# Optimization experiments

Hardware: AMD Instinct MI355X
Metric: run time of the kernel (lower is better)

## Reference

```python
import jax, jax.numpy as jnp
import numpy as np

S, P, H, E = 32, 32, 128, 64        # scenes, peds/scene, h_dim, embedding_dim
B1, B2 = 512, 1024                  # mlp_pre_pool hidden, bottleneck_dim
M1 = 1024                           # decoder mlp hidden
N = S * P
T = 12                              # seq_len (decode horizon)
BN_INV = 1.0 / np.sqrt(1.0 + 1e-5)  # eval-mode BatchNorm, running mean=0 var=1


def setup_inputs() -> dict:
    key = jax.random.key(0)
    ks = jax.random.split(key, 32)
    rn = lambda k, sh, s=0.05: jax.random.normal(k, sh, dtype=jnp.float32) * s
    inp = {
        'last_pos': rn(ks[0], (N, 2), 1.0),
        'last_pos_rel': rn(ks[1], (N, 2), 1.0),
        'h0': rn(ks[2], (N, H), 0.1),
        'c0': rn(ks[3], (N, H), 0.1),
        'seq_start_end': jnp.stack([jnp.arange(S) * P, (jnp.arange(S) + 1) * P], 1).astype(jnp.int32),
        # decoder spatial embedding Linear(2, E)
        'emb_W': rn(ks[4], (E, 2)), 'emb_b': rn(ks[5], (E,)),
        # LSTM (torch gate order i,f,g,o)
        'lstm_Wih': rn(ks[6], (4 * H, E)), 'lstm_Whh': rn(ks[7], (4 * H, H)),
        'lstm_bih': rn(ks[8], (4 * H,)), 'lstm_bhh': rn(ks[9], (4 * H,)),
        # hidden2pos Linear(H, 2)
        'pos_W': rn(ks[10], (2, H)), 'pos_b': rn(ks[11], (2,)),
        # pool_net spatial embedding Linear(2, E)
        'sp_W': rn(ks[12], (E, 2)), 'sp_b': rn(ks[13], (E,)),
        # mlp_pre_pool: Linear(E+H, 512)+BN+ReLU, Linear(512, 1024)+BN+ReLU
        'pp1_W': rn(ks[14], (B1, E + H)), 'pp1_b': rn(ks[15], (B1,)),
        'pp1_g': 1.0 + rn(ks[16], (B1,)), 'pp1_be': rn(ks[17], (B1,)),
        'pp2_W': rn(ks[18], (B2, B1)), 'pp2_b': rn(ks[19], (B2,)),
        'pp2_g': 1.0 + rn(ks[20], (B2,)), 'pp2_be': rn(ks[21], (B2,)),
        # decoder mlp: Linear(H+1024, 1024)+BN+ReLU, Linear(1024, H)+BN+ReLU
        'm1_W': rn(ks[22], (M1, H + B2)), 'm1_b': rn(ks[23], (M1,)),
        'm1_g': 1.0 + rn(ks[24], (M1,)), 'm1_be': rn(ks[25], (M1,)),
        'm2_W': rn(ks[26], (H, M1)), 'm2_b': rn(ks[27], (H,)),
        'm2_g': 1.0 + rn(ks[28], (H,)), 'm2_be': rn(ks[29], (H,)),
    }
    return inp


def _bn(x, g, b):
    return x * BN_INV * g + b


def reference(last_pos, last_pos_rel, h0, c0, seq_start_end,
              emb_W, emb_b, lstm_Wih, lstm_Whh, lstm_bih, lstm_bhh,
              pos_W, pos_b, sp_W, sp_b,
              pp1_W, pp1_b, pp1_g, pp1_be, pp2_W, pp2_b, pp2_g, pp2_be,
              m1_W, m1_b, m1_g, m1_be, m2_W, m2_b, m2_g, m2_be):
    # seq_start_end encodes uniform scenes of size P; pooling is done per scene.
    def step(carry, _):
        h, c, lp, din = carry  # h,c:[N,H]  lp:[N,2]  din:[N,E]
        gates = din @ lstm_Wih.T + lstm_bih + h @ lstm_Whh.T + lstm_bhh
        i, f, g_, o = jnp.split(gates, 4, axis=-1)
        c2 = jax.nn.sigmoid(f) * c + jax.nn.sigmoid(i) * jnp.tanh(g_)
        h2 = jax.nn.sigmoid(o) * jnp.tanh(c2)
        rel_pos = h2 @ pos_W.T + pos_b          # [N,2]
        curr = rel_pos + lp                     # [N,2]
        # ---- PoolHiddenNet: per-scene all-pairs gather -> MLP -> max ----
        ps = curr.reshape(S, P, 2)
        rel = ps[:, None, :, :] - ps[:, :, None, :]   # [s,i,j] = pos_j - pos_i
        rel = rel / jnp.maximum(jnp.linalg.norm(rel, axis=-1, keepdims=True), 1e-12)
        emb = rel @ sp_W.T + sp_b                      # [S,P,P,E]
        hj = jnp.broadcast_to(h2.reshape(S, 1, P, H), (S, P, P, H))
        x = jnp.concatenate([emb, hj], -1)             # [S,P,P,E+H]
        x = jax.nn.relu(_bn(x @ pp1_W.T + pp1_b, pp1_g, pp1_be))
        x = jax.nn.relu(_bn(x @ pp2_W.T + pp2_b, pp2_g, pp2_be))
        pool = x.max(axis=2).reshape(N, B2)            # max over neighbours j
        # ---- hidden refinement MLP ----
        dh = jnp.concatenate([h2, pool], 1)
        dh = jax.nn.relu(_bn(dh @ m1_W.T + m1_b, m1_g, m1_be))
        dh = jax.nn.relu(_bn(dh @ m2_W.T + m2_b, m2_g, m2_be))
        din2 = rel_pos @ emb_W.T + emb_b
        return (dh, c2, curr, din2), rel_pos

    din0 = last_pos_rel @ emb_W.T + emb_b
    _, preds = jax.lax.scan(step, (h0, c0, last_pos, din0), None, length=T)
    return preds  # [T, N, 2] predicted relative displacements
```

## Files before the change

### kernel.cpp

```cpp
#include <hip/hip_runtime.h>
#include <hip/hip_bf16.h>
#include <math.h>

#define DEVFN __device__ __forceinline__

constexpr float BN_INV = 0.99999500003749971f;

DEVFN float sigm(float x) { return 1.0f / (1.0f + expf(-x)); }

DEVFN unsigned short f2bf(float f) {
    __hip_bfloat16 b = __float2bfloat16(f);
    return *reinterpret_cast<unsigned short*>(&b);
}
DEVFN float bf2f(unsigned short u) {
    unsigned int x = ((unsigned int)u) << 16;
    return *reinterpret_cast<float*>(&x);
}
DEVFN void splitf(float v, unsigned short& h, unsigned short& l) {
    h = f2bf(v);
    l = f2bf(v - bf2f(h));
}
DEVFN unsigned int pack2(unsigned short a, unsigned short b) {
    return (unsigned int)a | ((unsigned int)b << 16);
}

typedef __attribute__((ext_vector_type(8))) short short8;
typedef __attribute__((ext_vector_type(4))) float f32x4;

#define ASYNC_COPY16(gsrc, ldst)                                                            \
    __builtin_amdgcn_global_load_lds((const __attribute__((address_space(1))) unsigned int*)(gsrc), \
                                     (__attribute__((address_space(3))) unsigned int*)(ldst), 16, 0, 0)


__global__ void pre_lstm(const float* __restrict__ Wih, const float* __restrict__ Whh,
                         const float* __restrict__ bih, const float* __restrict__ bhh,
                         float* __restrict__ WgT, float* __restrict__ bg) {
    int idx = blockIdx.x * blockDim.x + threadIdx.x;
    int k = idx >> 9, t = idx & 511;
    WgT[idx] = (k < 64) ? Wih[t * 64 + k] : Whh[t * 128 + (k - 64)];
    if (idx < 512) bg[idx] = bih[idx] + bhh[idx];
}

__global__ void pre_wh1(const float* __restrict__ pp1W, const float* __restrict__ pp1g,
                        float* __restrict__ Wh1T) {
    int idx = blockIdx.x * blockDim.x + threadIdx.x;
    int h = idx >> 9, k = idx & 511;
    Wh1T[idx] = pp1W[k * 192 + 64 + h] * (BN_INV * pp1g[k]);
}

__global__ void pre_mp(const float* __restrict__ spW, const float* __restrict__ spb,
                       const float* __restrict__ pp1W, const float* __restrict__ pp1b,
                       const float* __restrict__ pp1g, const float* __restrict__ pp1be,
                       float* __restrict__ Mp, float* __restrict__ c1) {
    int k = blockIdx.x * blockDim.x + threadIdx.x;
    float m0 = 0.f, m1 = 0.f, c0 = 0.f;
    for (int e = 0; e < 64; e++) {
        float w = pp1W[k * 192 + e];
        m0 += spW[e * 2] * w; m1 += spW[e * 2 + 1] * w; c0 += spb[e] * w;
    }
    float s = BN_INV * pp1g[k];
    Mp[k] = m0 * s; Mp[512 + k] = m1 * s;
    c1[k] = (c0 + pp1b[k]) * s + pp1be[k];
}

__global__ void pre_w2bf(const float* __restrict__ W, const float* __restrict__ b,
                         const float* __restrict__ g, const float* __restrict__ be,
                         unsigned short* __restrict__ Wbf, float* __restrict__ cv, int swz) {
    int idx = blockIdx.x * blockDim.x + threadIdx.x;
    int ko = idx >> 9, k = idx & 511;
    float s = BN_INV * g[ko];
    int outk = swz ? ((k & ~63) | ((((k >> 3) & 7) ^ (ko & 7)) << 3) | (k & 7)) : k;
    Wbf[(ko << 9) + outk] = f2bf(W[idx] * s);
    if (idx < 1024) cv[idx] = b[idx] * s + be[idx];
}

__global__ void pre_w1split(const float* __restrict__ W, const float* __restrict__ b,
                            const float* __restrict__ g, const float* __restrict__ be,
                            unsigned short* __restrict__ Wh, unsigned short* __restrict__ Wl,
                            float* __restrict__ cv) {
    int idx = blockIdx.x * blockDim.x + threadIdx.x;
    int ko = idx / 1152;
    float s = BN_INV * g[ko];
    unsigned short h, l;
    splitf(W[idx] * s, h, l);
    Wh[idx] = h; Wl[idx] = l;
    if (idx < 1024) {
        float s2 = BN_INV * g[idx];
        cv[idx] = b[idx] * s2 + be[idx];
    }
}

__global__ void pre_w2split(const float* __restrict__ W, const float* __restrict__ b,
                            const float* __restrict__ g, const float* __restrict__ be,
                            unsigned short* __restrict__ Wh, unsigned short* __restrict__ Wl,
                            float* __restrict__ cv) {
    int idx = blockIdx.x * blockDim.x + threadIdx.x;
    int ko = idx >> 10;
    float s = BN_INV * g[ko];
    unsigned short h, l;
    splitf(W[idx] * s, h, l);
    Wh[idx] = h; Wl[idx] = l;
    if (idx < 128) {
        float s2 = BN_INV * g[idx];
        cv[idx] = b[idx] * s2 + be[idx];
    }
}

__global__ void pre_init(const float* __restrict__ lp, const float* __restrict__ lpr,
                         const float* __restrict__ h0, const float* __restrict__ c0,
                         const float* __restrict__ embW, const float* __restrict__ embb,
                         float* __restrict__ h_st, float* __restrict__ c_st,
                         float* __restrict__ curr, float* __restrict__ din) {
    int idx = blockIdx.x * blockDim.x + threadIdx.x;
    h_st[idx] = h0[idx];
    c_st[idx] = c0[idx];
    if (idx < 1024 * 2) curr[idx] = lp[idx];
    if (idx < 1024 * 64) {
        int n = idx >> 6, e = idx & 63;
        din[idx] = fmaf(lpr[n * 2], embW[e * 2], fmaf(lpr[n * 2 + 1], embW[e * 2 + 1], embb[e]));
    }
}


__global__ __launch_bounds__(512) void k_lstm(
    const float* __restrict__ WgT, const float* __restrict__ bg,
    float* __restrict__ h_st, float* __restrict__ c_st,
    float* __restrict__ din, float* __restrict__ curr,
    unsigned short* __restrict__ h2h, unsigned short* __restrict__ h2l,
    const float* __restrict__ posW, const float* __restrict__ posb,
    const float* __restrict__ embW, const float* __restrict__ embb,
    const float* __restrict__ Wh1T, const float* __restrict__ c1,
    float* __restrict__ Hp, int doHp,
    float* __restrict__ preds) {
    int n0 = blockIdx.x << 2;
    int t = threadIdx.x;
    __shared__ float xs[4][256];
    __shared__ float gates[4][512];
    __shared__ float h2s[4][128];
    __shared__ float rp[4][2];
#pragma unroll
    for (int u = 0; u < 2; u++) {
        int lin = t + (u << 9);
        int r = lin >> 8, k = lin & 255;
        float v = 0.f;
        if (k < 64) v = din[(n0 + r) * 64 + k];
        else if (k < 192) v = h_st[(n0 + r) * 128 + (k - 64)];
        xs[r][k] = v;
    }
    __syncthreads();
    float a0 = bg[t], a1 = a0, a2 = a0, a3 = a0;
#pragma unroll 4
    for (int k = 0; k < 192; k++) {
        float w = WgT[(k << 9) + t];
        a0 = fmaf(xs[0][k], w, a0);
        a1 = fmaf(xs[1][k], w, a1);
        a2 = fmaf(xs[2][k], w, a2);
        a3 = fmaf(xs[3][k], w, a3);
    }
    gates[0][t] = a0; gates[1][t] = a1; gates[2][t] = a2; gates[3][t] = a3;
    __syncthreads();
    {
        int r = t >> 7, hx = t & 127;
        float ig = sigm(gates[r][hx]);
        float fg = sigm(gates[r][128 + hx]);
        float gg = tanhf(gates[r][256 + hx]);
        float og = sigm(gates[r][384 + hx]);
        float c2 = fmaf(fg, c_st[(n0 + r) * 128 + hx], ig * gg);
        float h2 = og * tanhf(c2);
        c_st[(n0 + r) * 128 + hx] = c2;
        unsigned short sh, sl;
        splitf(h2, sh, sl);
        h2h[(n0 + r) * 128 + hx] = sh;
        h2l[(n0 + r) * 128 + hx] = sl;
        h2s[r][hx] = h2;
    }
    __syncthreads();
    int wv = t >> 6, l = t & 63;
    if (wv < 4) {
        float p0 = fmaf(h2s[wv][l], posW[l], h2s[wv][l + 64] * posW[l + 64]);
        float p1 = fmaf(h2s[wv][l], posW[128 + l], h2s[wv][l + 64] * posW[192 + l]);
#pragma unroll
        for (int off = 32; off > 0; off >>= 1) {
            p0 += __shfl_down(p0, off, 64);
            p1 += __shfl_down(p1, off, 64);
        }
        if (l == 0) { rp[wv][0] = p0 + posb[0]; rp[wv][1] = p1 + posb[1]; }
    }
    __syncthreads();
    if (t < 256) {
        int r = t >> 6, e = t & 63;
        float r0 = rp[r][0], r1 = rp[r][1];
        din[(n0 + r) * 64 + e] = fmaf(r0, embW[e * 2], fmaf(r1, embW[e * 2 + 1], embb[e]));
        if (e == 0) {
            preds[(n0 + r) * 2] = r0; preds[(n0 + r) * 2 + 1] = r1;
            curr[(n0 + r) * 2] += r0; curr[(n0 + r) * 2 + 1] += r1;
        }
    }
    if (doHp) {
        float cc = c1[t];
        float q0 = cc, q1 = cc, q2 = cc, q3 = cc;
#pragma unroll 4
        for (int h = 0; h < 128; h++) {
            float w = Wh1T[(h << 9) + t];
            q0 = fmaf(h2s[0][h], w, q0);
            q1 = fmaf(h2s[1][h], w, q1);
            q2 = fmaf(h2s[2][h], w, q2);
            q3 = fmaf(h2s[3][h], w, q3);
        }
        Hp[((n0 + 0) << 9) + t] = q0;
        Hp[((n0 + 1) << 9) + t] = q1;
        Hp[((n0 + 2) << 9) + t] = q2;
        Hp[((n0 + 3) << 9) + t] = q3;
    }
}

__global__ __launch_bounds__(256) void k_x1(
    const float* __restrict__ Hp, const float* __restrict__ Mp,
    const float* __restrict__ curr, unsigned short* __restrict__ x1g) {
    int bid = blockIdx.x;
    int c = bid & 7, q = bid >> 3;
    int i = q & 31, g = q >> 5;
    int s = (g << 3) + c;
    int si = (s << 5) + i;
    int t = threadIdx.x;
    __shared__ float rx[32], ry[32];
    __shared__ float m0s[512], m1s[512];
    for (int u = t; u < 512; u += 256) { m0s[u] = Mp[u]; m1s[u] = Mp[512 + u]; }
    if (t < 32) {
        int jg = (s << 5) + t;
        float dx = curr[jg * 2] - curr[si * 2];
        float dy = curr[jg * 2 + 1] - curr[si * 2 + 1];
        float den = fmaxf(sqrtf(dx * dx + dy * dy), 1e-12f);
        rx[t] = dx / den; ry[t] = dy / den;
    }
    __syncthreads();
    int j = t >> 3, c8 = t & 7;
    float rxv = rx[j], ryv = ry[j];
    const float* hp = Hp + (((s << 5) + j) << 9);
    unsigned short* op = x1g + ((size_t)((si << 5) + j) << 9);
    int swz = (c8 ^ (j & 7)) << 3;
#pragma unroll
    for (int kt = 0; kt < 512; kt += 64) {
        int k = kt + (c8 << 3);
        float4 ha = *(const float4*)(hp + k);
        float4 hb = *(const float4*)(hp + k + 4);
        uint4 o;
        o.x = pack2(f2bf(fmaxf(fmaf(rxv, m0s[k + 0], fmaf(ryv, m1s[k + 0], ha.x)), 0.f)),
                    f2bf(fmaxf(fmaf(rxv, m0s[k + 1], fmaf(ryv, m1s[k + 1], ha.y)), 0.f)));
        o.y = pack2(f2bf(fmaxf(fmaf(rxv, m0s[k + 2], fmaf(ryv, m1s[k + 2], ha.z)), 0.f)),
                    f2bf(fmaxf(fmaf(rxv, m0s[k + 3], fmaf(ryv, m1s[k + 3], ha.w)), 0.f)));
        o.z = pack2(f2bf(fmaxf(fmaf(rxv, m0s[k + 4], fmaf(ryv, m1s[k + 4], hb.x)), 0.f)),
                    f2bf(fmaxf(fmaf(rxv, m0s[k + 5], fmaf(ryv, m1s[k + 5], hb.y)), 0.f)));
        o.w = pack2(f2bf(fmaxf(fmaf(rxv, m0s[k + 6], fmaf(ryv, m1s[k + 6], hb.z)), 0.f)),
                    f2bf(fmaxf(fmaf(rxv, m0s[k + 7], fmaf(ryv, m1s[k + 7], hb.w)), 0.f)));
        *(uint4*)(op + kt + swz) = o;
    }
}

__global__ __launch_bounds__(1024, 4) void k_pool_g(
    const unsigned short* __restrict__ x1g, const unsigned short* __restrict__ W2bf,
    const float* __restrict__ c2v,
    unsigned short* __restrict__ poolh, unsigned short* __restrict__ pooll) {
    int bid = blockIdx.x;
    int c = bid & 7, q = bid >> 3;
    int inner = q & 15, g = q >> 4;
    int s = (g << 3) + c;
    int rb = inner >> 2;
    int koB = (inner & 3) << 8;
    int t = threadIdx.x;
    int lane = t & 63, wv = t >> 6;
    int quad = lane >> 4, l15 = lane & 15;
    int wr = wv >> 2, wc = wv & 3;
    int qrow = wr << 6, qcol = wc << 6;
    __shared__ unsigned short As[256 * 64];
    __shared__ unsigned short Bs[256 * 64];
    f32x4 acc[4][4];
#pragma unroll
    for (int a = 0; a < 4; a++)
#pragma unroll
        for (int b = 0; b < 4; b++) acc[a][b] = (f32x4){0.f, 0.f, 0.f, 0.f};

    int rlane = lane >> 3;
    int clane = (lane & 7) << 3;
    const unsigned short* gA = x1g + (size_t)((s << 10) + (rb << 8) + (wv << 4) + rlane) * 512 + clane;
    const unsigned short* gB = W2bf + (size_t)(koB + (wv << 4) + rlane) * 512 + clane;
    unsigned short* lA = As + (wv << 10);
    unsigned short* lB = Bs + (wv << 10);
    const unsigned short* pa0 = As + ((qrow + l15) << 6) + ((quad ^ (l15 & 7)) << 3);
    const unsigned short* pb0 = Bs + ((qcol + l15) << 6) + ((quad ^ (l15 & 7)) << 3);
    const unsigned short* pa1 = As + ((qrow + l15) << 6) + (((4 + quad) ^ (l15 & 7)) << 3);
    const unsigned short* pb1 = Bs + ((qcol + l15) << 6) + (((4 + quad) ^ (l15 & 7)) << 3);

    for (int kt = 0; kt < 512; kt += 64) {
        ASYNC_COPY16(gA + kt, lA);
        ASYNC_COPY16(gA + kt + 8 * 512, lA + (8 << 6));
        ASYNC_COPY16(gB + kt, lB);
        ASYNC_COPY16(gB + kt + 8 * 512, lB + (8 << 6));
        __syncthreads();
        {
            short8 aF[4], bF[4];
#pragma unroll
            for (int a = 0; a < 4; a++) aF[a] = *(const short8*)(pa0 + (a << 10));
#pragma unroll
            for (int b = 0; b < 4; b++) bF[b] = *(const short8*)(pb0 + (b << 10));
#pragma unroll
            for (int a = 0; a < 4; a++)
#pragma unroll
                for (int b = 0; b < 4; b++)
                    acc[a][b] = __builtin_amdgcn_mfma_f32_16x16x32_bf16(aF[a], bF[b], acc[a][b], 0, 0, 0);
#pragma unroll
            for (int a = 0; a < 4; a++) aF[a] = *(const short8*)(pa1 + (a << 10));
#pragma unroll
            for (int b = 0; b < 4; b++) bF[b] = *(const short8*)(pb1 + (b << 10));
#pragma unroll
            for (int a = 0; a < 4; a++)
#pragma unroll
                for (int b = 0; b < 4; b++)
                    acc[a][b] = __builtin_amdgcn_mfma_f32_16x16x32_bf16(aF[a], bF[b], acc[a][b], 0, 0, 0);
        }
        __syncthreads();
    }

    float mx0[4], mx1[4];
#pragma unroll
    for (int b = 0; b < 4; b++) {
        float m = acc[0][b].x;
#pragma unroll
        for (int a = 0; a < 2; a++) {
            m = fmaxf(m, acc[a][b].x); m = fmaxf(m, acc[a][b].y);
            m = fmaxf(m, acc[a][b].z); m = fmaxf(m, acc[a][b].w);
        }
        m = fmaxf(m, __shfl_xor(m, 16));
        m = fmaxf(m, __shfl_xor(m, 32));
        mx0[b] = m;
        float n = acc[2][b].x;
#pragma unroll
        for (int a = 2; a < 4; a++) {
            n = fmaxf(n, acc[a][b].x); n = fmaxf(n, acc[a][b].y);
            n = fmaxf(n, acc[a][b].z); n = fmaxf(n, acc[a][b].w);
        }
        n = fmaxf(n, __shfl_xor(n, 16));
        n = fmaxf(n, __shfl_xor(n, 32));
        mx1[b] = n;
    }
    float v0 = (quad == 0) ? mx0[0] : (quad == 1) ? mx0[1] : (quad == 2) ? mx0[2] : mx0[3];
    float v1 = (quad == 0) ? mx1[0] : (quad == 1) ? mx1[1] : (quad == 2) ? mx1[2] : mx1[3];
    int col = koB + qcol + (quad << 4) + l15;
    int i0 = (rb << 3) + (wr << 1);
    int si0 = (s << 5) + i0;
    float bias = c2v[col];
    float w0 = fmaxf(v0 + bias, 0.f);
    float w1 = fmaxf(v1 + bias, 0.f);
    unsigned short h0, l0, h1, l1;
    splitf(w0, h0, l0); splitf(w1, h1, l1);
    poolh[si0 * 1024 + col] = h0; pooll[si0 * 1024 + col] = l0;
    poolh[(si0 + 1) * 1024 + col] = h1; pooll[(si0 + 1) * 1024 + col] = l1;
}

__global__ __launch_bounds__(256) void k_pool_mfma(
    const float* __restrict__ Hp, const float* __restrict__ Mp,
    const unsigned short* __restrict__ W2bf,
    const float* __restrict__ c2v, const float* __restrict__ curr,
    unsigned short* __restrict__ poolh, unsigned short* __restrict__ pooll) {
    int s = blockIdx.z;
    int rb = blockIdx.y;
    int koBase = blockIdx.x << 7;
    int t = threadIdx.x;
    int lane = t & 63, wv = t >> 6;
    int quad = lane >> 4, l15 = lane & 15;
    int qrow = (wv >> 1) << 6;
    int qcol = (wv & 1) << 6;

    __shared__ unsigned short As[128 * 40];
    __shared__ unsigned short Bs[128 * 40];
    __shared__ float rx[128], ry[128];

    if (t < 128) {
        int iL = t >> 5, j = t & 31;
        int ig = (s << 5) + (rb << 2) + iL;
        int jg = (s << 5) + j;
        float dx = curr[jg * 2] - curr[ig * 2];
        float dy = curr[jg * 2 + 1] - curr[ig * 2 + 1];
        float den = fmaxf(sqrtf(dx * dx + dy * dy), 1e-12f);
        rx[t] = dx / den; ry[t] = dy / den;
    }
    __syncthreads();

    f32x4 acc[4][4];
#pragma unroll
    for (int a = 0; a < 4; a++)
#pragma unroll
        for (int b = 0; b < 4; b++) acc[a][b] = (f32x4){0.f, 0.f, 0.f, 0.f};

    int r0 = t >> 3, c4 = (t & 7) << 2;
    int bn = t >> 1, bk = (t & 1) << 4;

    for (int kt = 0; kt < 512; kt += 32) {
#pragma unroll
        for (int p = 0; p < 4; p++) {
            int rr = r0 + (p << 5);
            int j = rr & 31;
            int kg = kt + c4;
            float4 hv = *(const float4*)(Hp + (((s << 5) + j) << 9) + kg);
            float4 m0 = *(const float4*)(Mp + kg);
            float4 m1 = *(const float4*)(Mp + 512 + kg);
            float rxv = rx[rr], ryv = ry[rr];
            float v0 = fmaxf(fmaf(rxv, m0.x, fmaf(ryv, m1.x, hv.x)), 0.f);
            float v1 = fmaxf(fmaf(rxv, m0.y, fmaf(ryv, m1.y, hv.y)), 0.f);
            float v2 = fmaxf(fmaf(rxv, m0.z, fmaf(ryv, m1.z, hv.z)), 0.f);
            float v3 = fmaxf(fmaf(rxv, m0.w, fmaf(ryv, m1.w, hv.w)), 0.f);
            unsigned int u0 = pack2(f2bf(v0), f2bf(v1));
            unsigned int u1 = pack2(f2bf(v2), f2bf(v3));
            *(uint2*)(&As[rr * 40 + c4]) = make_uint2(u0, u1);
        }
        {
            const unsigned short* src = W2bf + (((koBase + bn) << 9) + kt + bk);
            uint4 w0 = *(const uint4*)src;
            uint4 w1 = *(const uint4*)(src + 8);
            *(uint4*)(&Bs[bn * 40 + bk]) = w0;
            *(uint4*)(&Bs[bn * 40 + bk + 8]) = w1;
        }
        __syncthreads();
        short8 bF[4];
#pragma unroll
        for (int b = 0; b < 4; b++)
            bF[b] = *(const short8*)(&Bs[(qcol + (b << 4) + l15) * 40 + (quad << 3)]);
#pragma unroll
        for (int a = 0; a < 4; a++) {
            short8 aF = *(const short8*)(&As[(qrow + (a << 4) + l15) * 40 + (quad << 3)]);
#pragma unroll
            for (int b = 0; b < 4; b++)
                acc[a][b] = __builtin_amdgcn_mfma_f32_16x16x32_bf16(aF, bF[b], acc[a][b], 0, 0, 0);
        }
        __syncthreads();
    }

    float mx0[4], mx1[4];
#pragma unroll
    for (int b = 0; b < 4; b++) {
        float m = acc[0][b].x;
#pragma unroll
        for (int a = 0; a < 2; a++) {
            m = fmaxf(m, acc[a][b].x); m = fmaxf(m, acc[a][b].y);
            m = fmaxf(m, acc[a][b].z); m = fmaxf(m, acc[a][b].w);
        }
        m = fmaxf(m, __shfl_xor(m, 16));
        m = fmaxf(m, __shfl_xor(m, 32));
        mx0[b] = m;
        float n = acc[2][b].x;
#pragma unroll
        for (int a = 2; a < 4; a++) {
            n = fmaxf(n, acc[a][b].x); n = fmaxf(n, acc[a][b].y);
            n = fmaxf(n, acc[a][b].z); n = fmaxf(n, acc[a][b].w);
        }
        n = fmaxf(n, __shfl_xor(n, 16));
        n = fmaxf(n, __shfl_xor(n, 32));
        mx1[b] = n;
    }
    float v0 = (quad == 0) ? mx0[0] : (quad == 1) ? mx0[1] : (quad == 2) ? mx0[2] : mx0[3];
    float v1 = (quad == 0) ? mx1[0] : (quad == 1) ? mx1[1] : (quad == 2) ? mx1[2] : mx1[3];
    int col = koBase + qcol + (quad << 4) + l15;
    int i0 = (rb << 2) + ((wv >> 1) << 1);
    int si0 = (s << 5) + i0;
    float bias = c2v[col];
    float w0 = fmaxf(v0 + bias, 0.f);
    float w1 = fmaxf(v1 + bias, 0.f);
    unsigned short h0, l0, h1, l1;
    splitf(w0, h0, l0); splitf(w1, h1, l1);
    poolh[si0 * 1024 + col] = h0; pooll[si0 * 1024 + col] = l0;
    poolh[(si0 + 1) * 1024 + col] = h1; pooll[(si0 + 1) * 1024 + col] = l1;
}

__global__ __launch_bounds__(256) void k_m1_mfma(
    const unsigned short* __restrict__ h2h, const unsigned short* __restrict__ h2l,
    const unsigned short* __restrict__ poolh, const unsigned short* __restrict__ pooll,
    const unsigned short* __restrict__ M1h, const unsigned short* __restrict__ M1l,
    const float* __restrict__ cm1,
    unsigned short* __restrict__ dh1h, unsigned short* __restrict__ dh1l) {
    int rowBase = blockIdx.y << 6;
    int koBase = blockIdx.x << 6;
    int t = threadIdx.x;
    int lane = t & 63, wv = t >> 6;
    int quad = lane >> 4, l15 = lane & 15;
    int qrow = (wv >> 1) << 5, qcol = (wv & 1) << 5;
    __shared__ unsigned short Ah[64 * 40], Al[64 * 40], Bh[64 * 40], Bl[64 * 40];
    f32x4 acc[2][2];
#pragma unroll
    for (int a = 0; a < 2; a++)
#pragma unroll
        for (int b = 0; b < 2; b++) acc[a][b] = (f32x4){0.f, 0.f, 0.f, 0.f};

    int ar = t >> 2, ak = (t & 3) << 3;

    for (int kt = 0; kt < 1152; kt += 32) {
        {
            const unsigned short* sH;
            const unsigned short* sL;
            int off;
            if (kt < 128) {
                off = (rowBase + ar) * 128 + kt + ak;
                sH = h2h; sL = h2l;
            } else {
                off = (rowBase + ar) * 1024 + (kt - 128) + ak;
                sH = poolh; sL = pooll;
            }
            *(uint4*)&Ah[ar * 40 + ak] = *(const uint4*)(sH + off);
            *(uint4*)&Al[ar * 40 + ak] = *(const uint4*)(sL + off);
        }
        {
            int boff = (koBase + ar) * 1152 + kt + ak;
            *(uint4*)&Bh[ar * 40 + ak] = *(const uint4*)(M1h + boff);
            *(uint4*)&Bl[ar * 40 + ak] = *(const uint4*)(M1l + boff);
        }
        __syncthreads();
        short8 bH[2], bL[2];
#pragma unroll
        for (int b = 0; b < 2; b++) {
            int boff = (qcol + (b << 4) + l15) * 40 + (quad << 3);
            bH[b] = *(const short8*)(&Bh[boff]);
            bL[b] = *(const short8*)(&Bl[boff]);
        }
#pragma unroll
        for (int a = 0; a < 2; a++) {
            int aoff = (qrow + (a << 4) + l15) * 40 + (quad << 3);
            short8 aH = *(const short8*)(&Ah[aoff]);
            short8 aL = *(const short8*)(&Al[aoff]);
#pragma unroll
            for (int b = 0; b < 2; b++) {
                acc[a][b] = __builtin_amdgcn_mfma_f32_16x16x32_bf16(aH, bH[b], acc[a][b], 0, 0, 0);
                acc[a][b] = __builtin_amdgcn_mfma_f32_16x16x32_bf16(aH, bL[b], acc[a][b], 0, 0, 0);
                acc[a][b] = __builtin_amdgcn_mfma_f32_16x16x32_bf16(aL, bH[b], acc[a][b], 0, 0, 0);
            }
        }
        __syncthreads();
    }
#pragma unroll
    for (int b = 0; b < 2; b++) {
        int col = koBase + qcol + (b << 4) + l15;
        float bias = cm1[col];
#pragma unroll
        for (int a = 0; a < 2; a++) {
#pragma unroll
            for (int rg = 0; rg < 4; rg++) {
                int row = rowBase + qrow + (a << 4) + (quad << 2) + rg;
                float v = fmaxf(acc[a][b][rg] + bias, 0.f);
                unsigned short sh, sl;
                splitf(v, sh, sl);
                dh1h[row * 1024 + col] = sh;
                dh1l[row * 1024 + col] = sl;
            }
        }
    }
}

__global__ __launch_bounds__(256) void k_m2_mfma(
    const unsigned short* __restrict__ dh1h, const unsigned short* __restrict__ dh1l,
    const unsigned short* __restrict__ M2h, const unsigned short* __restrict__ M2l,
    const float* __restrict__ cm2, float* __restrict__ h_st) {
    int rowBase = blockIdx.x << 6;
    int t = threadIdx.x;
    int lane = t & 63, wv = t >> 6;
    int quad = lane >> 4, l15 = lane & 15;
    int qrow = (wv >> 1) << 5;
    int qcol = (wv & 1) << 6;
    __shared__ unsigned short Ah[64 * 40], Al[64 * 40], Bh[128 * 40], Bl[128 * 40];
    f32x4 acc[2][4];
#pragma unroll
    for (int a = 0; a < 2; a++)
#pragma unroll
        for (int b = 0; b < 4; b++) acc[a][b] = (f32x4){0.f, 0.f, 0.f, 0.f};

    int ar = t >> 2, ak = (t & 3) << 3;
    int br = t >> 1, bk = (t & 1) << 4;

    for (int kt = 0; kt < 1024; kt += 32) {
        {
            int off = (rowBase + ar) * 1024 + kt + ak;
            *(uint4*)&Ah[ar * 40 + ak] = *(const uint4*)(dh1h + off);
            *(uint4*)&Al[ar * 40 + ak] = *(const uint4*)(dh1l + off);
        }
        {
            int off = br * 1024 + kt + bk;
            *(uint4*)&Bh[br * 40 + bk] = *(const uint4*)(M2h + off);
            *(uint4*)&Bh[br * 40 + bk + 8] = *(const uint4*)(M2h + off + 8);
            *(uint4*)&Bl[br * 40 + bk] = *(const uint4*)(M2l + off);
            *(uint4*)&Bl[br * 40 + bk + 8] = *(const uint4*)(M2l + off + 8);
        }
        __syncthreads();
#pragma unroll
        for (int a = 0; a < 2; a++) {
            int aoff = (qrow + (a << 4) + l15) * 40 + (quad << 3);
            short8 aH = *(const short8*)(&Ah[aoff]);
            short8 aL = *(const short8*)(&Al[aoff]);
#pragma unroll
            for (int b = 0; b < 4; b++) {
                int boff = (qcol + (b << 4) + l15) * 40 + (quad << 3);
                short8 bH = *(const short8*)(&Bh[boff]);
                short8 bL = *(const short8*)(&Bl[boff]);
                acc[a][b] = __builtin_amdgcn_mfma_f32_16x16x32_bf16(aH, bH, acc[a][b], 0, 0, 0);
                acc[a][b] = __builtin_amdgcn_mfma_f32_16x16x32_bf16(aH, bL, acc[a][b], 0, 0, 0);
                acc[a][b] = __builtin_amdgcn_mfma_f32_16x16x32_bf16(aL, bH, acc[a][b], 0, 0, 0);
            }
        }
        __syncthreads();
    }
#pragma unroll
    for (int b = 0; b < 4; b++) {
        int col = qcol + (b << 4) + l15;
        float bias = cm2[col];
#pragma unroll
        for (int a = 0; a < 2; a++) {
#pragma unroll
            for (int rg = 0; rg < 4; rg++) {
                int row = rowBase + qrow + (a << 4) + (quad << 2) + rg;
                h_st[row * 128 + col] = fmaxf(acc[a][b][rg] + bias, 0.f);
            }
        }
    }
}


extern "C" void kernel_launch(void* const* d_in, const int* in_sizes, int n_in,
                              void* d_out, int out_size, void* d_ws, size_t ws_size,
                              hipStream_t stream) {
    const float* last_pos     = (const float*)d_in[0];
    const float* last_pos_rel = (const float*)d_in[1];
    const float* h0   = (const float*)d_in[2];
    const float* c0   = (const float*)d_in[3];
    const float* emb_W = (const float*)d_in[5];
    const float* emb_b = (const float*)d_in[6];
    const float* lstm_Wih = (const float*)d_in[7];
    const float* lstm_Whh = (const float*)d_in[8];
    const float* lstm_bih = (const float*)d_in[9];
    const float* lstm_bhh = (const float*)d_in[10];
    const float* pos_W = (const float*)d_in[11];
    const float* pos_b = (const float*)d_in[12];
    const float* sp_W  = (const float*)d_in[13];
    const float* sp_b  = (const float*)d_in[14];
    const float* pp1_W = (const float*)d_in[15];
    const float* pp1_b = (const float*)d_in[16];
    const float* pp1_g = (const float*)d_in[17];
    const float* pp1_be= (const float*)d_in[18];
    const float* pp2_W = (const float*)d_in[19];
    const float* pp2_b = (const float*)d_in[20];
    const float* pp2_g = (const float*)d_in[21];
    const float* pp2_be= (const float*)d_in[22];
    const float* m1_W  = (const float*)d_in[23];
    const float* m1_b  = (const float*)d_in[24];
    const float* m1_g  = (const float*)d_in[25];
    const float* m1_be = (const float*)d_in[26];
    const float* m2_W  = (const float*)d_in[27];
    const float* m2_b  = (const float*)d_in[28];
    const float* m2_g  = (const float*)d_in[29];
    const float* m2_be = (const float*)d_in[30];
    float* out = (float*)d_out;

    float* p = (float*)d_ws;
    float* WgT  = p; p += 192 * 512;
    float* bg   = p; p += 512;
    float* Wh1T = p; p += 128 * 512;
    float* Mp   = p; p += 2 * 512;
    float* c1   = p; p += 512;
    unsigned short* W2bf = (unsigned short*)p; p += 512 * 1024 / 2;
    float* c2v  = p; p += 1024;
    unsigned short* M1h = (unsigned short*)p; p += 1024 * 1152 / 2;
    unsigned short* M1l = (unsigned short*)p; p += 1024 * 1152 / 2;
    float* cm1  = p; p += 1024;
    unsigned short* M2h = (unsigned short*)p; p += 128 * 1024 / 2;
    unsigned short* M2l = (unsigned short*)p; p += 128 * 1024 / 2;
    float* cm2  = p; p += 128;
    float* h_st = p; p += 1024 * 128;
    float* c_st = p; p += 1024 * 128;
    unsigned short* h2h = (unsigned short*)p; p += 1024 * 128 / 2;
    unsigned short* h2l = (unsigned short*)p; p += 1024 * 128 / 2;
    float* curr = p; p += 1024 * 2;
    float* din  = p; p += 1024 * 64;
    float* Hp   = p; p += 1024 * 512;
    unsigned short* poolh = (unsigned short*)p; p += 1024 * 1024 / 2;
    unsigned short* pooll = (unsigned short*)p; p += 1024 * 1024 / 2;
    unsigned short* dh1h = (unsigned short*)p; p += 1024 * 1024 / 2;
    unsigned short* dh1l = (unsigned short*)p; p += 1024 * 1024 / 2;
    unsigned short* x1g = (unsigned short*)p;
    size_t need = (size_t)((char*)(x1g + (size_t)32768 * 512) - (char*)d_ws);
    int big = (ws_size >= need) ? 1 : 0;

    pre_lstm<<<384, 256, 0, stream>>>(lstm_Wih, lstm_Whh, lstm_bih, lstm_bhh, WgT, bg);
    pre_wh1<<<256, 256, 0, stream>>>(pp1_W, pp1_g, Wh1T);
    pre_mp<<<2, 256, 0, stream>>>(sp_W, sp_b, pp1_W, pp1_b, pp1_g, pp1_be, Mp, c1);
    pre_w2bf<<<2048, 256, 0, stream>>>(pp2_W, pp2_b, pp2_g, pp2_be, W2bf, c2v, big);
    pre_w1split<<<4608, 256, 0, stream>>>(m1_W, m1_b, m1_g, m1_be, M1h, M1l, cm1);
    pre_w2split<<<512, 256, 0, stream>>>(m2_W, m2_b, m2_g, m2_be, M2h, M2l, cm2);
    pre_init<<<512, 256, 0, stream>>>(last_pos, last_pos_rel, h0, c0, emb_W, emb_b,
                                      h_st, c_st, curr, din);

    for (int t = 0; t < 12; t++) {
        k_lstm<<<256, 512, 0, stream>>>(WgT, bg, h_st, c_st, din, curr, h2h, h2l,
                                        pos_W, pos_b, emb_W, emb_b,
                                        Wh1T, c1, Hp, (t < 11) ? 1 : 0, out + t * 2048);
        if (t == 11) break;
        if (big) {
            k_x1<<<1024, 256, 0, stream>>>(Hp, Mp, curr, x1g);
            k_pool_g<<<512, 1024, 0, stream>>>(x1g, W2bf, c2v, poolh, pooll);
        } else {
            k_pool_mfma<<<dim3(8, 8, 32), 256, 0, stream>>>(Hp, Mp, W2bf, c2v, curr,
                                                            poolh, pooll);
        }
        k_m1_mfma<<<dim3(16, 16), 256, 0, stream>>>(h2h, h2l, poolh, pooll,
                                                    M1h, M1l, cm1, dh1h, dh1l);
        k_m2_mfma<<<16, 256, 0, stream>>>(dh1h, dh1l, M2h, M2l, cm2, h_st);
    }
}
```

Baseline: 1.517 ms.

## Double-buffer pool GEMM, widen m1 K-tile, split m2 rows, merge prep kernels

Several unrelated changes land together. The pool GEMM kernel double-buffers its LDS tiles so the async global-to-LDS copy of the next K-slice overlaps the MFMAs on the current one, with one barrier per iteration instead of two. The m1 GEMM now loads a 64-wide K tile per iteration, halving the loop trips and barriers. The m2 GEMM uses 32-row blocks to launch twice as many workgroups, and four small setup kernels are merged into one launch. The costs are doubled LDS in k_pool_g, which at 1024 threads may cut occupancy, and more shared memory in the m1 kernel.

```diff
diff --git a/kernel.cpp b/kernel.cpp
--- a/kernel.cpp
+++ b/kernel.cpp
@@ -32,35 +32,50 @@
                                      (__attribute__((address_space(3))) unsigned int*)(ldst), 16, 0, 0)
 
 
-__global__ void pre_lstm(const float* __restrict__ Wih, const float* __restrict__ Whh,
-                         const float* __restrict__ bih, const float* __restrict__ bhh,
-                         float* __restrict__ WgT, float* __restrict__ bg) {
-    int idx = blockIdx.x * blockDim.x + threadIdx.x;
-    int k = idx >> 9, t = idx & 511;
-    WgT[idx] = (k < 64) ? Wih[t * 64 + k] : Whh[t * 128 + (k - 64)];
-    if (idx < 512) bg[idx] = bih[idx] + bhh[idx];
-}
-
-__global__ void pre_wh1(const float* __restrict__ pp1W, const float* __restrict__ pp1g,
-                        float* __restrict__ Wh1T) {
-    int idx = blockIdx.x * blockDim.x + threadIdx.x;
-    int h = idx >> 9, k = idx & 511;
-    Wh1T[idx] = pp1W[k * 192 + 64 + h] * (BN_INV * pp1g[k]);
-}
-
-__global__ void pre_mp(const float* __restrict__ spW, const float* __restrict__ spb,
-                       const float* __restrict__ pp1W, const float* __restrict__ pp1b,
-                       const float* __restrict__ pp1g, const float* __restrict__ pp1be,
-                       float* __restrict__ Mp, float* __restrict__ c1) {
-    int k = blockIdx.x * blockDim.x + threadIdx.x;
-    float m0 = 0.f, m1 = 0.f, c0 = 0.f;
-    for (int e = 0; e < 64; e++) {
-        float w = pp1W[k * 192 + e];
-        m0 += spW[e * 2] * w; m1 += spW[e * 2 + 1] * w; c0 += spb[e] * w;
-    }
-    float s = BN_INV * pp1g[k];
-    Mp[k] = m0 * s; Mp[512 + k] = m1 * s;
-    c1[k] = (c0 + pp1b[k]) * s + pp1be[k];
+__global__ void pre_misc(
+    const float* __restrict__ Wih, const float* __restrict__ Whh,
+    const float* __restrict__ bih, const float* __restrict__ bhh,
+    float* __restrict__ WgT, float* __restrict__ bg,
+    const float* __restrict__ pp1W, const float* __restrict__ pp1g,
+    float* __restrict__ Wh1T,
+    const float* __restrict__ spW, const float* __restrict__ spb,
+    const float* __restrict__ pp1b, const float* __restrict__ pp1be,
+    float* __restrict__ Mp, float* __restrict__ c1,
+    const float* __restrict__ lp, const float* __restrict__ lpr,
+    const float* __restrict__ h0, const float* __restrict__ c0,
+    const float* __restrict__ embW, const float* __restrict__ embb,
+    float* __restrict__ h_st, float* __restrict__ c_st,
+    float* __restrict__ curr, float* __restrict__ din) {
+    int bid = blockIdx.x, t = threadIdx.x;
+    if (bid < 384) {
+        int idx = bid * 256 + t;
+        int k = idx >> 9, tt = idx & 511;
+        WgT[idx] = (k < 64) ? Wih[tt * 64 + k] : Whh[tt * 128 + (k - 64)];
+        if (idx < 512) bg[idx] = bih[idx] + bhh[idx];
+    } else if (bid < 640) {
+        int idx = (bid - 384) * 256 + t;
+        int h = idx >> 9, k = idx & 511;
+        Wh1T[idx] = pp1W[k * 192 + 64 + h] * (BN_INV * pp1g[k]);
+    } else if (bid < 642) {
+        int k = (bid - 640) * 256 + t;
+        float m0 = 0.f, m1 = 0.f, c0v = 0.f;
+        for (int e = 0; e < 64; e++) {
+            float w = pp1W[k * 192 + e];
+            m0 += spW[e * 2] * w; m1 += spW[e * 2 + 1] * w; c0v += spb[e] * w;
+        }
+        float s = BN_INV * pp1g[k];
+        Mp[k] = m0 * s; Mp[512 + k] = m1 * s;
+        c1[k] = (c0v + pp1b[k]) * s + pp1be[k];
+    } else {
+        int idx = (bid - 642) * 256 + t;
+        h_st[idx] = h0[idx];
+        c_st[idx] = c0[idx];
+        if (idx < 1024 * 2) curr[idx] = lp[idx];
+        if (idx < 1024 * 64) {
+            int n = idx >> 6, e = idx & 63;
+            din[idx] = fmaf(lpr[n * 2], embW[e * 2], fmaf(lpr[n * 2 + 1], embW[e * 2 + 1], embb[e]));
+        }
+    }
 }
 
 __global__ void pre_w2bf(const float* __restrict__ W, const float* __restrict__ b,
@@ -103,21 +118,6 @@
     if (idx < 128) {
         float s2 = BN_INV * g[idx];
         cv[idx] = b[idx] * s2 + be[idx];
-    }
-}
-
-__global__ void pre_init(const float* __restrict__ lp, const float* __restrict__ lpr,
-                         const float* __restrict__ h0, const float* __restrict__ c0,
-                         const float* __restrict__ embW, const float* __restrict__ embb,
-                         float* __restrict__ h_st, float* __restrict__ c_st,
-                         float* __restrict__ curr, float* __restrict__ din) {
-    int idx = blockIdx.x * blockDim.x + threadIdx.x;
-    h_st[idx] = h0[idx];
-    c_st[idx] = c0[idx];
-    if (idx < 1024 * 2) curr[idx] = lp[idx];
-    if (idx < 1024 * 64) {
-        int n = idx >> 6, e = idx & 63;
-        din[idx] = fmaf(lpr[n * 2], embW[e * 2], fmaf(lpr[n * 2 + 1], embW[e * 2 + 1], embb[e]));
     }
 }
 
@@ -272,8 +272,8 @@
     int quad = lane >> 4, l15 = lane & 15;
     int wr = wv >> 2, wc = wv & 3;
     int qrow = wr << 6, qcol = wc << 6;
-    __shared__ unsigned short As[256 * 64];
-    __shared__ unsigned short Bs[256 * 64];
+    __shared__ unsigned short As[2][256 * 64];
+    __shared__ unsigned short Bs[2][256 * 64];
     f32x4 acc[4][4];
 #pragma unroll
     for (int a = 0; a < 4; a++)
@@ -284,42 +284,48 @@
     int clane = (lane & 7) << 3;
     const unsigned short* gA = x1g + (size_t)((s << 10) + (rb << 8) + (wv << 4) + rlane) * 512 + clane;
     const unsigned short* gB = W2bf + (size_t)(koB + (wv << 4) + rlane) * 512 + clane;
-    unsigned short* lA = As + (wv << 10);
-    unsigned short* lB = Bs + (wv << 10);
-    const unsigned short* pa0 = As + ((qrow + l15) << 6) + ((quad ^ (l15 & 7)) << 3);
-    const unsigned short* pb0 = Bs + ((qcol + l15) << 6) + ((quad ^ (l15 & 7)) << 3);
-    const unsigned short* pa1 = As + ((qrow + l15) << 6) + (((4 + quad) ^ (l15 & 7)) << 3);
-    const unsigned short* pb1 = Bs + ((qcol + l15) << 6) + (((4 + quad) ^ (l15 & 7)) << 3);
-
-    for (int kt = 0; kt < 512; kt += 64) {
-        ASYNC_COPY16(gA + kt, lA);
-        ASYNC_COPY16(gA + kt + 8 * 512, lA + (8 << 6));
-        ASYNC_COPY16(gB + kt, lB);
-        ASYNC_COPY16(gB + kt + 8 * 512, lB + (8 << 6));
+    const unsigned short* pa0 = &As[0][((qrow + l15) << 6) + ((quad ^ (l15 & 7)) << 3)];
+    const unsigned short* pb0 = &Bs[0][((qcol + l15) << 6) + ((quad ^ (l15 & 7)) << 3)];
+    const unsigned short* pa1 = &As[0][((qrow + l15) << 6) + (((4 + quad) ^ (l15 & 7)) << 3)];
+    const unsigned short* pb1 = &Bs[0][((qcol + l15) << 6) + (((4 + quad) ^ (l15 & 7)) << 3)];
+
+#define POOL_STAGE(kt, buf)                                           \
+    do {                                                              \
+        unsigned short* lA = &As[buf][wv << 10];                      \
+        unsigned short* lB = &Bs[buf][wv << 10];                      \
+        ASYNC_COPY16(gA + (kt), lA);                                  \
+        ASYNC_COPY16(gA + (kt) + 8 * 512, lA + (8 << 6));             \
+        ASYNC_COPY16(gB + (kt), lB);                                  \
+        ASYNC_COPY16(gB + (kt) + 8 * 512, lB + (8 << 6));             \
+    } while (0)
+
+    POOL_STAGE(0, 0);
+    __syncthreads();
+    for (int i = 0; i < 8; i++) {
+        if (i < 7) POOL_STAGE((i + 1) << 6, (i + 1) & 1);
+        int off = (i & 1) << 14;
+        short8 aF[4], bF[4];
+#pragma unroll
+        for (int a = 0; a < 4; a++) aF[a] = *(const short8*)(pa0 + off + (a << 10));
+#pragma unroll
+        for (int b = 0; b < 4; b++) bF[b] = *(const short8*)(pb0 + off + (b << 10));
+#pragma unroll
+        for (int a = 0; a < 4; a++)
+#pragma unroll
+            for (int b = 0; b < 4; b++)
+                acc[a][b] = __builtin_amdgcn_mfma_f32_16x16x32_bf16(aF[a], bF[b], acc[a][b], 0, 0, 0);
+#pragma unroll
+        for (int a = 0; a < 4; a++) aF[a] = *(const short8*)(pa1 + off + (a << 10));
+#pragma unroll
+        for (int b = 0; b < 4; b++) bF[b] = *(const short8*)(pb1 + off + (b << 10));
+#pragma unroll
+        for (int a = 0; a < 4; a++)
+#pragma unroll
+            for (int b = 0; b < 4; b++)
+                acc[a][b] = __builtin_amdgcn_mfma_f32_16x16x32_bf16(aF[a], bF[b], acc[a][b], 0, 0, 0);
         __syncthreads();
-        {
-            short8 aF[4], bF[4];
-#pragma unroll
-            for (int a = 0; a < 4; a++) aF[a] = *(const short8*)(pa0 + (a << 10));
-#pragma unroll
-            for (int b = 0; b < 4; b++) bF[b] = *(const short8*)(pb0 + (b << 10));
-#pragma unroll
-            for (int a = 0; a < 4; a++)
-#pragma unroll
-                for (int b = 0; b < 4; b++)
-                    acc[a][b] = __builtin_amdgcn_mfma_f32_16x16x32_bf16(aF[a], bF[b], acc[a][b], 0, 0, 0);
-#pragma unroll
-            for (int a = 0; a < 4; a++) aF[a] = *(const short8*)(pa1 + (a << 10));
-#pragma unroll
-            for (int b = 0; b < 4; b++) bF[b] = *(const short8*)(pb1 + (b << 10));
-#pragma unroll
-            for (int a = 0; a < 4; a++)
-#pragma unroll
-                for (int b = 0; b < 4; b++)
-                    acc[a][b] = __builtin_amdgcn_mfma_f32_16x16x32_bf16(aF[a], bF[b], acc[a][b], 0, 0, 0);
-        }
-        __syncthreads();
-    }
+    }
+#undef POOL_STAGE
 
     float mx0[4], mx1[4];
 #pragma unroll
@@ -483,16 +489,16 @@
     int lane = t & 63, wv = t >> 6;
     int quad = lane >> 4, l15 = lane & 15;
     int qrow = (wv >> 1) << 5, qcol = (wv & 1) << 5;
-    __shared__ unsigned short Ah[64 * 40], Al[64 * 40], Bh[64 * 40], Bl[64 * 40];
+    __shared__ unsigned short Ah[64 * 72], Al[64 * 72], Bh[64 * 72], Bl[64 * 72];
     f32x4 acc[2][2];
 #pragma unroll
     for (int a = 0; a < 2; a++)
 #pragma unroll
         for (int b = 0; b < 2; b++) acc[a][b] = (f32x4){0.f, 0.f, 0.f, 0.f};
 
-    int ar = t >> 2, ak = (t & 3) << 3;
-
-    for (int kt = 0; kt < 1152; kt += 32) {
+    int ar = t >> 2, ak = (t & 3) << 4;
+
+    for (int kt = 0; kt < 1152; kt += 64) {
         {
             const unsigned short* sH;
             const unsigned short* sL;
@@ -504,32 +510,40 @@
                 off = (rowBase + ar) * 1024 + (kt - 128) + ak;
                 sH = poolh; sL = pooll;
             }
-            *(uint4*)&Ah[ar * 40 + ak] = *(const uint4*)(sH + off);
-            *(uint4*)&Al[ar * 40 + ak] = *(const uint4*)(sL + off);
+            *(uint4*)&Ah[ar * 72 + ak] = *(const uint4*)(sH + off);
+            *(uint4*)&Ah[ar * 72 + ak + 8] = *(const uint4*)(sH + off + 8);
+            *(uint4*)&Al[ar * 72 + ak] = *(const uint4*)(sL + off);
+            *(uint4*)&Al[ar * 72 + ak + 8] = *(const uint4*)(sL + off + 8);
         }
         {
             int boff = (koBase + ar) * 1152 + kt + ak;
-            *(uint4*)&Bh[ar * 40 + ak] = *(const uint4*)(M1h + boff);
-            *(uint4*)&Bl[ar * 40 + ak] = *(const uint4*)(M1l + boff);
+            *(uint4*)&Bh[ar * 72 + ak] = *(const uint4*)(M1h + boff);
+            *(uint4*)&Bh[ar * 72 + ak + 8] = *(const uint4*)(M1h + boff + 8);
+            *(uint4*)&Bl[ar * 72 + ak] = *(const uint4*)(M1l + boff);
+            *(uint4*)&Bl[ar * 72 + ak + 8] = *(const uint4*)(M1l + boff + 8);
         }
         __syncthreads();
-        short8 bH[2], bL[2];
-#pragma unroll
-        for (int b = 0; b < 2; b++) {
-            int boff = (qcol + (b << 4) + l15) * 40 + (quad << 3);
-            bH[b] = *(const short8*)(&Bh[boff]);
-            bL[b] = *(const short8*)(&Bl[boff]);
-        }
-#pragma unroll
-        for (int a = 0; a < 2; a++) {
-            int aoff = (qrow + (a << 4) + l15) * 40 + (quad << 3);
-            short8 aH = *(const short8*)(&Ah[aoff]);
-            short8 aL = *(const short8*)(&Al[aoff]);
+#pragma unroll
+        for (int kk2 = 0; kk2 < 2; kk2++) {
+            int kc = ((kk2 << 2) | quad) << 3;
+            short8 bH[2], bL[2];
 #pragma unroll
             for (int b = 0; b < 2; b++) {
-                acc[a][b] = __builtin_amdgcn_mfma_f32_16x16x32_bf16(aH, bH[b], acc[a][b], 0, 0, 0);
-                acc[a][b] = __builtin_amdgcn_mfma_f32_16x16x32_bf16(aH, bL[b], acc[a][b], 0, 0, 0);
-                acc[a][b] = __builtin_amdgcn_mfma_f32_16x16x32_bf16(aL, bH[b], acc[a][b], 0, 0, 0);
+                int boff = (qcol + (b << 4) + l15) * 72 + kc;
+                bH[b] = *(const short8*)(&Bh[boff]);
+                bL[b] = *(const short8*)(&Bl[boff]);
+            }
+#pragma unroll
+            for (int a = 0; a < 2; a++) {
+                int aoff = (qrow + (a << 4) + l15) * 72 + kc;
+                short8 aH = *(const short8*)(&Ah[aoff]);
+                short8 aL = *(const short8*)(&Al[aoff]);
+#pragma unroll
+                for (int b = 0; b < 2; b++) {
+                    acc[a][b] = __builtin_amdgcn_mfma_f32_16x16x32_bf16(aH, bH[b], acc[a][b], 0, 0, 0);
+                    acc[a][b] = __builtin_amdgcn_mfma_f32_16x16x32_bf16(aH, bL[b], acc[a][b], 0, 0, 0);
+                    acc[a][b] = __builtin_amdgcn_mfma_f32_16x16x32_bf16(aL, bH[b], acc[a][b], 0, 0, 0);
+                }
             }
         }
         __syncthreads();
@@ -557,27 +571,25 @@
     const unsigned short* __restrict__ dh1h, const unsigned short* __restrict__ dh1l,
     const unsigned short* __restrict__ M2h, const unsigned short* __restrict__ M2l,
     const float* __restrict__ cm2, float* __restrict__ h_st) {
-    int rowBase = blockIdx.x << 6;
+    int rowBase = blockIdx.x << 5;
     int t = threadIdx.x;
     int lane = t & 63, wv = t >> 6;
     int quad = lane >> 4, l15 = lane & 15;
-    int qrow = (wv >> 1) << 5;
+    int qrow = (wv >> 1) << 4;
     int qcol = (wv & 1) << 6;
-    __shared__ unsigned short Ah[64 * 40], Al[64 * 40], Bh[128 * 40], Bl[128 * 40];
-    f32x4 acc[2][4];
-#pragma unroll
-    for (int a = 0; a < 2; a++)
-#pragma unroll
-        for (int b = 0; b < 4; b++) acc[a][b] = (f32x4){0.f, 0.f, 0.f, 0.f};
-
-    int ar = t >> 2, ak = (t & 3) << 3;
+    __shared__ unsigned short Ah[32 * 40], Al[32 * 40], Bh[128 * 40], Bl[128 * 40];
+    f32x4 acc[4];
+#pragma unroll
+    for (int b = 0; b < 4; b++) acc[b] = (f32x4){0.f, 0.f, 0.f, 0.f};
+
+    int ar = t >> 3, ak = (t & 7) << 2;
     int br = t >> 1, bk = (t & 1) << 4;
 
     for (int kt = 0; kt < 1024; kt += 32) {
         {
             int off = (rowBase + ar) * 1024 + kt + ak;
-            *(uint4*)&Ah[ar * 40 + ak] = *(const uint4*)(dh1h + off);
-            *(uint4*)&Al[ar * 40 + ak] = *(const uint4*)(dh1l + off);
+            *(uint2*)&Ah[ar * 40 + ak] = *(const uint2*)(dh1h + off);
+            *(uint2*)&Al[ar * 40 + ak] = *(const uint2*)(dh1l + off);
         }
         {
             int off = br * 1024 + kt + bk;
@@ -587,9 +599,8 @@
             *(uint4*)&Bl[br * 40 + bk + 8] = *(const uint4*)(M2l + off + 8);
         }
         __syncthreads();
-#pragma unroll
-        for (int a = 0; a < 2; a++) {
-            int aoff = (qrow + (a << 4) + l15) * 40 + (quad << 3);
+        {
+            int aoff = (qrow + l15) * 40 + (quad << 3);
             short8 aH = *(const short8*)(&Ah[aoff]);
             short8 aL = *(const short8*)(&Al[aoff]);
 #pragma unroll
@@ -597,9 +608,9 @@
                 int boff = (qcol + (b << 4) + l15) * 40 + (quad << 3);
                 short8 bH = *(const short8*)(&Bh[boff]);
                 short8 bL = *(const short8*)(&Bl[boff]);
-                acc[a][b] = __builtin_amdgcn_mfma_f32_16x16x32_bf16(aH, bH, acc[a][b], 0, 0, 0);
-                acc[a][b] = __builtin_amdgcn_mfma_f32_16x16x32_bf16(aH, bL, acc[a][b], 0, 0, 0);
-                acc[a][b] = __builtin_amdgcn_mfma_f32_16x16x32_bf16(aL, bH, acc[a][b], 0, 0, 0);
+                acc[b] = __builtin_amdgcn_mfma_f32_16x16x32_bf16(aH, bH, acc[b], 0, 0, 0);
+                acc[b] = __builtin_amdgcn_mfma_f32_16x16x32_bf16(aH, bL, acc[b], 0, 0, 0);
+                acc[b] = __builtin_amdgcn_mfma_f32_16x16x32_bf16(aL, bH, acc[b], 0, 0, 0);
             }
         }
         __syncthreads();
@@ -609,12 +620,9 @@
         int col = qcol + (b << 4) + l15;
         float bias = cm2[col];
 #pragma unroll
-        for (int a = 0; a < 2; a++) {
-#pragma unroll
-            for (int rg = 0; rg < 4; rg++) {
-                int row = rowBase + qrow + (a << 4) + (quad << 2) + rg;
-                h_st[row * 128 + col] = fmaxf(acc[a][b][rg] + bias, 0.f);
-            }
+        for (int rg = 0; rg < 4; rg++) {
+            int row = rowBase + qrow + (quad << 2) + rg;
+            h_st[row * 128 + col] = fmaxf(acc[b][rg] + bias, 0.f);
         }
     }
 }
@@ -684,14 +692,14 @@
     size_t need = (size_t)((char*)(x1g + (size_t)32768 * 512) - (char*)d_ws);
     int big = (ws_size >= need) ? 1 : 0;
 
-    pre_lstm<<<384, 256, 0, stream>>>(lstm_Wih, lstm_Whh, lstm_bih, lstm_bhh, WgT, bg);
-    pre_wh1<<<256, 256, 0, stream>>>(pp1_W, pp1_g, Wh1T);
-    pre_mp<<<2, 256, 0, stream>>>(sp_W, sp_b, pp1_W, pp1_b, pp1_g, pp1_be, Mp, c1);
+    pre_misc<<<1154, 256, 0, stream>>>(lstm_Wih, lstm_Whh, lstm_bih, lstm_bhh, WgT, bg,
+                                       pp1_W, pp1_g, Wh1T,
+                                       sp_W, sp_b, pp1_b, pp1_be, Mp, c1,
+                                       last_pos, last_pos_rel, h0, c0, emb_W, emb_b,
+                                       h_st, c_st, curr, din);
     pre_w2bf<<<2048, 256, 0, stream>>>(pp2_W, pp2_b, pp2_g, pp2_be, W2bf, c2v, big);
     pre_w1split<<<4608, 256, 0, stream>>>(m1_W, m1_b, m1_g, m1_be, M1h, M1l, cm1);
     pre_w2split<<<512, 256, 0, stream>>>(m2_W, m2_b, m2_g, m2_be, M2h, M2l, cm2);
-    pre_init<<<512, 256, 0, stream>>>(last_pos, last_pos_rel, h0, c0, emb_W, emb_b,
-                                      h_st, c_st, curr, din);
 
     for (int t = 0; t < 12; t++) {
         k_lstm<<<256, 512, 0, stream>>>(WgT, bg, h_st, c_st, din, curr, h2h, h2l,
@@ -707,6 +715,6 @@
         }
         k_m1_mfma<<<dim3(16, 16), 256, 0, stream>>>(h2h, h2l, poolh, pooll,
                                                     M1h, M1l, cm1, dh1h, dh1l);
-        k_m2_mfma<<<16, 256, 0, stream>>>(dh1h, dh1l, M2h, M2l, cm2, h_st);
-    }
-}
+        k_m2_mfma<<<32, 256, 0, stream>>>(dh1h, dh1l, M2h, M2l, cm2, h_st);
+    }
+}
```

After: 1.387 ms. 8.6% less time.
